# Kernel tuning notes

Measured on AMD Instinct MI355X. Metric: run time of the kernel, lower is better.

## Reference

```python
import jax, jax.numpy as jnp
import numpy as np

B, S = 32, 48
H, W_IMG, DEPTH = 48, 72, 1
UNITS, MOTOR, SENSORY = 48, 4, 1283
ODE_UNFOLDS = 6
N_ACTIONS = 2
EPS = 1e-8


def setup_inputs() -> dict:
    key = jax.random.key(0)
    ks = jax.random.split(key, 32)
    inp = {}
    inp["image"] = jax.random.uniform(ks[0], (B, S, DEPTH, H, W_IMG), jnp.float32)
    inp["rel_pos"] = jax.random.normal(ks[1], (B, S, 3), jnp.float32)
    # CNN params: channels [1->32->64->32], k=3, stride=2, VALID
    dims = [DEPTH, 32, 64, 32]
    for i in range(3):
        fan_in = dims[i] * 9
        inp[f"w{i}"] = jax.random.normal(ks[2 + i], (dims[i + 1], dims[i], 3, 3), jnp.float32) / np.sqrt(fan_in)
        inp[f"b{i}"] = jnp.zeros((dims[i + 1],), jnp.float32)
    # LTC input affine mapping
    inp["input_w"] = jnp.ones((SENSORY,), jnp.float32)
    inp["input_b"] = jnp.zeros((SENSORY,), jnp.float32)
    # LTC neuron params (ncps default init ranges)
    u = lambda k, shp, lo, hi: jax.random.uniform(k, shp, jnp.float32, lo, hi)
    inp["gleak"] = u(ks[6], (UNITS,), 0.001, 1.0)
    inp["vleak"] = u(ks[7], (UNITS,), -0.2, 0.2)
    inp["cm"] = u(ks[8], (UNITS,), 0.4, 0.6)
    # recurrent synapse params [pre=UNITS, post=UNITS]
    inp["sigma"] = u(ks[9], (UNITS, UNITS), 3.0, 8.0)
    inp["mu"] = u(ks[10], (UNITS, UNITS), 0.3, 0.8)
    inp["w_syn"] = u(ks[11], (UNITS, UNITS), 0.001, 1.0)
    inp["erev"] = (2.0 * jax.random.randint(ks[12], (UNITS, UNITS), 0, 2).astype(jnp.float32) - 1.0)
    # sensory synapse params [pre=SENSORY, post=UNITS]
    inp["s_sigma"] = u(ks[13], (SENSORY, UNITS), 3.0, 8.0)
    inp["s_mu"] = u(ks[14], (SENSORY, UNITS), 0.3, 0.8)
    inp["s_w"] = u(ks[15], (SENSORY, UNITS), 0.001, 1.0)
    inp["s_erev"] = (2.0 * jax.random.randint(ks[16], (SENSORY, UNITS), 0, 2).astype(jnp.float32) - 1.0)
    # output affine mapping over the 4 motor neurons
    inp["w_out"] = jnp.ones((MOTOR,), jnp.float32)
    inp["b_out"] = jnp.zeros((MOTOR,), jnp.float32)
    # actor head: Linear(4 -> n_actions) + tanh
    inp["w_head"] = jax.random.normal(ks[17], (MOTOR, N_ACTIONS), jnp.float32) / np.sqrt(MOTOR)
    inp["b_head"] = jnp.zeros((N_ACTIONS,), jnp.float32)
    # sparsity masks (buffers, non-trainable): AutoNCP-like sparse wiring
    inp["syn_mask"] = jax.random.randint(ks[18], (UNITS, UNITS), 0, 2, jnp.int32)
    inp["sens_mask"] = (jax.random.uniform(ks[19], (SENSORY, UNITS)) < 0.4).astype(jnp.int32)
    return inp


def _cnn(x, w0, b0, w1, b1, w2, b2):
    # x: [N, C, H, W], VALID padding, stride 2, ReLU
    for w, b in ((w0, b0), (w1, b1), (w2, b2)):
        x = jax.lax.conv_general_dilated(x, w, (2, 2), "VALID",
                                         dimension_numbers=("NCHW", "OIHW", "NCHW"))
        x = jax.nn.relu(x + b[None, :, None, None])
    return x


def _ltc(xs, input_w, input_b, gleak, vleak, cm, sigma, mu, w_syn, erev,
         s_sigma, s_mu, s_w, s_erev, w_out, b_out, syn_mask_f, sens_mask_f):
    # xs: [B, S, SENSORY] -> outputs [B, S, MOTOR]
    xs = xs * input_w + input_b  # input affine mapping
    cm_t = cm * ODE_UNFOLDS      # cm / (elapsed_time / ode_unfolds), elapsed=1

    def cell(v, x_t):
        # sensory synapse activation, computed once per step: [B, SENSORY, UNITS]
        sa = s_w * jax.nn.sigmoid((x_t[:, :, None] - s_mu) * s_sigma) * sens_mask_f
        w_num_s = jnp.sum(sa * s_erev, axis=1)  # [B, UNITS]
        w_den_s = jnp.sum(sa, axis=1)
        for _ in range(ODE_UNFOLDS):
            # recurrent synapse activation: [B, UNITS(pre), UNITS(post)]
            wa = w_syn * jax.nn.sigmoid((v[:, :, None] - mu) * sigma) * syn_mask_f
            num = cm_t * v + gleak * vleak + jnp.sum(wa * erev, axis=1) + w_num_s
            den = cm_t + gleak + jnp.sum(wa, axis=1) + w_den_s + EPS
            v = num / den
        out = v[:, :MOTOR] * w_out + b_out  # motor neurons + output affine
        return v, out

    v0 = jnp.zeros((xs.shape[0], UNITS), xs.dtype)
    _, outs = jax.lax.scan(cell, v0, jnp.swapaxes(xs, 0, 1))  # scan over time
    return jnp.swapaxes(outs, 0, 1)  # [B, S, MOTOR]


def reference(image, rel_pos, w0, b0, w1, b1, w2, b2, input_w, input_b,
              gleak, vleak, cm, sigma, mu, w_syn, erev,
              s_sigma, s_mu, s_w, s_erev, w_out, b_out, w_head, b_head,
              syn_mask, sens_mask):
    b, s = image.shape[0], image.shape[1]
    img = image.reshape(b * s, *image.shape[2:])
    feat = _cnn(img, w0, b0, w1, b1, w2, b2).reshape(b, s, -1)  # [B,S,1280]
    x = jnp.concatenate([feat, rel_pos.reshape(b, s, -1)], axis=2)  # [B,S,1283]
    outs = _ltc(x, input_w, input_b, gleak, vleak, cm, sigma, mu, w_syn, erev,
                s_sigma, s_mu, s_w, s_erev, w_out, b_out,
                syn_mask.astype(x.dtype), sens_mask.astype(x.dtype))
    pooled = outs.mean(axis=1)  # [B, MOTOR]
    return jnp.tanh(pooled @ w_head + b_head)  # [B, N_ACTIONS]
```

## Files before the change

### kernel.cpp

```cpp
#include <hip/hip_runtime.h>
#include <math.h>

#define DINL __device__ __forceinline__

typedef __attribute__((ext_vector_type(8))) short short8;
typedef __attribute__((ext_vector_type(4))) float f32x4;
typedef unsigned short ushortx;
typedef unsigned int uintx;


static constexpr int O_OUT2 = 0;
static constexpr int O_X    = O_OUT2 + 1536 * 187 * 64;
static constexpr int O_WNUM = O_X + 1536 * 1283;
static constexpr int O_WDEN = O_WNUM + 1536 * 48;
static constexpr int O_SP4  = O_WDEN + 1536 * 48;
static constexpr int O_WM   = O_SP4 + 4 * 48 * 1283;
static constexpr int O_WME  = O_WM + 48 * 48;
static constexpr int O_W2T  = O_WME + 48 * 48;
static constexpr int O_W1H  = O_W2T + 32 * 9 * 64;
static constexpr int O_W1L  = O_W1H + 9216;

DINL float sigmoid_f(float z) {
  return __builtin_amdgcn_rcpf(1.f + __expf(-z));
}

DINL ushortx bf16_rne(float x) {
  uintx u = __float_as_uint(x);
  return (ushortx)((u + 0x7FFFu + ((u >> 16) & 1u)) >> 16);
}

__global__ __launch_bounds__(256) void k_pre(
    const float* __restrict__ ssig, const float* __restrict__ smu,
    const float* __restrict__ sw, const float* __restrict__ serev,
    const int* __restrict__ smask,
    const float* __restrict__ w_syn, const float* __restrict__ erev,
    const int* __restrict__ syn_mask,
    const float* __restrict__ w1, const float* __restrict__ w2,
    float4* __restrict__ o_p4, float* __restrict__ o_wm, float* __restrict__ o_wme,
    float* __restrict__ w2t, ushortx* __restrict__ w1h, ushortx* __restrict__ w1l) {
  const int bid = blockIdx.x, t = threadIdx.x;
  if (bid < 241) {
    int idx = bid * 256 + t;
    if (idx < 61584) {
      int i = idx / 48, j = idx - i * 48;
      float m = (float)smask[idx];
      float w = sw[idx] * m;
      o_p4[j * 1283 + i] = make_float4(ssig[idx], smu[idx], w, w * serev[idx]);
    }
  } else if (bid < 250) {
    int idx = (bid - 241) * 256 + t;
    if (idx < 2304) {
      float wm = w_syn[idx] * (float)syn_mask[idx];
      o_wm[idx]  = wm;
      o_wme[idx] = wm * erev[idx];
    }
  } else {
    int idx = (bid - 250) * 256 + t;
    if (idx < 18432) {
      int oc = idx / 288;
      int rem = idx - oc * 288;
      int c = rem / 9, k = rem - c * 9;
      float v = w1[idx];
      ushortx h = bf16_rne(v);
      float hv = __uint_as_float(((uintx)h) << 16);
      ushortx l = bf16_rne(v - hv);
      int dst = (k * 64 + oc) * 32 + c;
      w1h[dst] = h;
      w1l[dst] = l;
    } else if (idx < 36864) {
      int i2 = idx - 18432;
      int oc = i2 / 576;
      int rem = i2 - oc * 576;
      int c = rem / 9, k = rem - c * 9;
      w2t[(((oc & 15) * 9 + k) * 64 + c) * 2 + (oc >> 4)] = w2[i2];
    }
  }
}

__global__ __launch_bounds__(512) void k_conv12(const float* __restrict__ gimg,
        const float* __restrict__ w0, const float* __restrict__ b0,
        const ushortx* __restrict__ w1h, const ushortx* __restrict__ w1l,
        const float* __restrict__ b1, float* __restrict__ gout2) {
  extern __shared__ __align__(16) char dyn[];
  ushortx* c1h = (ushortx*)dyn;
  ushortx* c1l = c1h + 26496;
  float* smem_a = (float*)(c1l + 26496);
  float* sw0 = smem_a + 3456;
  float* sb0 = sw0 + 288;
  ushortx* swh = (ushortx*)smem_a;
  ushortx* swl = swh + 2048;

  const int n = blockIdx.x, t = threadIdx.x;

  const float* gi = gimg + n * 3456;
  for (int k = t; k < 3456; k += 512) smem_a[k] = gi[k];
  if (t < 288) sw0[t] = w0[t];
  if (t >= 480) sb0[t - 480] = b0[t - 480];

  const int lane = t & 63, wid = t >> 6;
  const int r15 = lane & 15, kg = lane >> 4;
  const int mt0 = (wid & 1) * 2;
  const int nt0 = (wid >> 1) * 3;
  int bbase[3], spv[3];
#pragma unroll
  for (int ni = 0; ni < 3; ++ni) {
    int sp = (nt0 + ni) * 16 + r15;
    spv[ni] = sp;
    int spc = sp > 186 ? 186 : sp;
    int oh = spc / 17, ow = spc - oh * 17;
    bbase[ni] = ((2 * oh) * 36 + 2 * ow) * 32 + kg * 8;
  }
  int aoff0 = (mt0 * 16 + r15) * 32 + kg * 8;
  float4 bb[2];
  bb[0] = *(const float4*)(b1 + mt0 * 16 + kg * 4);
  bb[1] = *(const float4*)(b1 + (mt0 + 1) * 16 + kg * 4);
  f32x4 acc[2][3];
#pragma unroll
  for (int mi = 0; mi < 2; ++mi)
#pragma unroll
    for (int ni = 0; ni < 3; ++ni) acc[mi][ni] = (f32x4)(0.f);

  __syncthreads();

  for (int idx = t; idx < 25760; idx += 512) {
    int c = idx & 31, sp = idx >> 5;
    int oh = sp / 35, ow = sp - oh * 35;
    const float* ip = smem_a + (2 * oh) * 72 + 2 * ow;
    const float* wp = sw0 + c * 9;
    float a = sb0[c];
#pragma unroll
    for (int kh = 0; kh < 3; ++kh)
      a += ip[kh * 72 + 0] * wp[kh * 3 + 0] + ip[kh * 72 + 1] * wp[kh * 3 + 1]
         + ip[kh * 72 + 2] * wp[kh * 3 + 2];
    a = fmaxf(a, 0.f);
    ushortx h = bf16_rne(a);
    float hv = __uint_as_float(((uintx)h) << 16);
    ushortx l = bf16_rne(a - hv);
    int pos = (oh * 36 + ow) * 32 + c;
    c1h[pos] = h;
    c1l[pos] = l;
  }

  const uintx* gwh = (const uintx*)w1h;
  const uintx* gwl = (const uintx*)w1l;
  for (int tap = 0; tap < 9; ++tap) {
    __syncthreads();
    for (int k = t; k < 1024; k += 512) {
      ((uintx*)swh)[k] = gwh[tap * 1024 + k];
      ((uintx*)swl)[k] = gwl[tap * 1024 + k];
    }
    __syncthreads();
    const int kh = tap / 3, kw = tap - kh * 3;
    const int toff = (kh * 36 + kw) * 32;
    short8 ah[2], al[2];
    ah[0] = *(const short8*)(swh + aoff0);
    al[0] = *(const short8*)(swl + aoff0);
    ah[1] = *(const short8*)(swh + aoff0 + 512);
    al[1] = *(const short8*)(swl + aoff0 + 512);
#pragma unroll
    for (int ni = 0; ni < 3; ++ni) {
      short8 bh = *(const short8*)(c1h + bbase[ni] + toff);
      short8 bl = *(const short8*)(c1l + bbase[ni] + toff);
#pragma unroll
      for (int mi = 0; mi < 2; ++mi) {
        acc[mi][ni] = __builtin_amdgcn_mfma_f32_16x16x32_bf16(ah[mi], bh, acc[mi][ni], 0, 0, 0);
        acc[mi][ni] = __builtin_amdgcn_mfma_f32_16x16x32_bf16(al[mi], bh, acc[mi][ni], 0, 0, 0);
        acc[mi][ni] = __builtin_amdgcn_mfma_f32_16x16x32_bf16(ah[mi], bl, acc[mi][ni], 0, 0, 0);
      }
    }
  }

  float* go = gout2 + n * 11968;
#pragma unroll
  for (int mi = 0; mi < 2; ++mi)
#pragma unroll
    for (int ni = 0; ni < 3; ++ni) {
      if (spv[ni] < 187) {
        float4 v;
        v.x = fmaxf(acc[mi][ni][0] + bb[mi].x, 0.f);
        v.y = fmaxf(acc[mi][ni][1] + bb[mi].y, 0.f);
        v.z = fmaxf(acc[mi][ni][2] + bb[mi].z, 0.f);
        v.w = fmaxf(acc[mi][ni][3] + bb[mi].w, 0.f);
        *(float4*)(go + spv[ni] * 64 + (mt0 + mi) * 16 + kg * 4) = v;
      }
    }
}

__global__ __launch_bounds__(256, 4) void k_conv3(const float* __restrict__ gout2,
        const float* __restrict__ w2t, const float* __restrict__ b2,
        const float* __restrict__ grel, float* __restrict__ gx) {
  __shared__ __align__(16) float sin2g[16 * 198];
  __shared__ __align__(16) float sw2g[16 * 290];
  const int n = blockIdx.x, t = threadIdx.x;
  const float* gi = gout2 + n * 11968;

  const int oc = t & 15, g = t >> 4;
  float acc[3][2];
  int rowb[3];
#pragma unroll
  for (int q = 0; q < 3; ++q) {
    acc[q][0] = b2[oc]; acc[q][1] = b2[oc + 16];
    int sp = q * 16 + g; if (sp > 39) sp = 39;
    int oh = sp >> 3, ow = sp & 7;
    rowb[q] = (2 * oh) * 18 + 2 * ow;
  }

  for (int grp = 0; grp < 4; ++grp) {
    for (int idx = t; idx < 2992; idx += 256) {
      int sp = idx >> 4, c = idx & 15;
      int h = sp / 17, w = sp - h * 17;
      sin2g[c * 198 + h * 18 + w] = gi[sp * 64 + grp * 16 + c];
    }
    for (int idx = t; idx < 4608; idx += 256) {
      int ocq2 = idx / 288, r = idx - ocq2 * 288;
      int k = r >> 5;
      sw2g[ocq2 * 290 + r] = w2t[(ocq2 * 9 + k) * 128 + grp * 32 + (r & 31)];
    }
    __syncthreads();

    for (int c = 0; c < 16; ++c) {
      const float* cb = sin2g + c * 198;
      const float* wb = sw2g + oc * 290 + c * 2;
#pragma unroll
      for (int kh = 0; kh < 3; ++kh) {
        float2 wv0 = *(const float2*)(wb + (kh * 3 + 0) * 32);
        float2 wv1 = *(const float2*)(wb + (kh * 3 + 1) * 32);
        float2 wv2 = *(const float2*)(wb + (kh * 3 + 2) * 32);
#pragma unroll
        for (int q = 0; q < 3; ++q) {
          const float* p = cb + rowb[q] + kh * 18;
          float2 x01 = *(const float2*)p;
          float x2 = p[2];
          acc[q][0] += x01.x * wv0.x + x01.y * wv1.x + x2 * wv2.x;
          acc[q][1] += x01.x * wv0.y + x01.y * wv1.y + x2 * wv2.y;
        }
      }
    }
    __syncthreads();
  }

  float* xo = gx + n * 1283;
#pragma unroll
  for (int q = 0; q < 3; ++q) {
    int sp = q * 16 + g;
    if (sp < 40) {
      xo[oc * 40 + sp]        = fmaxf(acc[q][0], 0.f);
      xo[(oc + 16) * 40 + sp] = fmaxf(acc[q][1], 0.f);
    }
  }
  if (t < 3) xo[1280 + t] = grel[n * 3 + t];
}

__global__ __launch_bounds__(256) void k_sensory(const float* __restrict__ gx,
        const float* __restrict__ iw, const float* __restrict__ ib,
        const float4* __restrict__ p4,
        float* __restrict__ wnum, float* __restrict__ wden) {
  __shared__ float xs[4 * 1283];
  const int t = threadIdx.x, bid = blockIdx.x;
  const int bs0 = (bid >> 1) * 4;
  const int jbase = (bid & 1) * 24;
  for (int idx = t; idx < 4 * 1283; idx += 256) {
    int slot = idx / 1283, i = idx - slot * 1283;
    xs[idx] = gx[(bs0 + slot) * 1283 + i] * iw[i] + ib[i];
  }
  __syncthreads();
  const int w = t >> 6, l = t & 63;
  for (int jj = 0; jj < 6; ++jj) {
    int j = jbase + w * 6 + jj;
    const float4* pp = p4 + j * 1283;
    float an[4], ad[4];
#pragma unroll
    for (int s2 = 0; s2 < 4; ++s2) { an[s2] = 0.f; ad[s2] = 0.f; }
    for (int i = l; i < 1283; i += 64) {
      float4 P = pp[i];
#pragma unroll
      for (int s2 = 0; s2 < 4; ++s2) {
        float sg = sigmoid_f((xs[s2 * 1283 + i] - P.y) * P.x);
        an[s2] += P.w * sg;
        ad[s2] += P.z * sg;
      }
    }
#pragma unroll
    for (int off = 32; off; off >>= 1)
#pragma unroll
      for (int s2 = 0; s2 < 4; ++s2) {
        an[s2] += __shfl_xor(an[s2], off);
        ad[s2] += __shfl_xor(ad[s2], off);
      }
    if (l == 0) {
#pragma unroll
      for (int s2 = 0; s2 < 4; ++s2) {
        wnum[(bs0 + s2) * 48 + j] = an[s2];
        wden[(bs0 + s2) * 48 + j] = ad[s2];
      }
    }
  }
}

__global__ __launch_bounds__(384) void k_scan(const float* __restrict__ gmu,
        const float* __restrict__ gsig, const float* __restrict__ wm,
        const float* __restrict__ wme, const float* __restrict__ wnum,
        const float* __restrict__ wden, const float* __restrict__ gleak,
        const float* __restrict__ vleak, const float* __restrict__ cm,
        const float* __restrict__ w_out, const float* __restrict__ b_out,
        const float* __restrict__ w_head, const float* __restrict__ b_head,
        float* __restrict__ out) {
  __shared__ float4 sp4[48 * 49];
  __shared__ float vbuf[2][48];
  __shared__ float m4[4];
  const int t = threadIdx.x, b = blockIdx.x;
  for (int idx = t; idx < 2304; idx += 384) {
    int i = idx / 48, jx = idx - i * 48;
    sp4[i * 49 + jx] = make_float4(gmu[idx], gsig[idx], wm[idx], wme[idx]);
  }
  if (t < 48) { vbuf[0][t] = 0.f; vbuf[1][t] = 0.f; }
  __syncthreads();

  const int j = t >> 3, g = t & 7;
  const float cmt = cm[j] * 6.f;
  const float gl = gleak[j];
  const float glv = gl * vleak[j];
  float psum = 0.f;
  const float* pn = wnum + b * 2304 + j;
  const float* pd = wden + b * 2304 + j;

  for (int s = 0; s < 48; ++s) {
    float wns = pn[s * 48], wds = pd[s * 48];
#pragma unroll 1
    for (int u = 0; u < 6; ++u) {
      int cur = u & 1;
      float an = 0.f, ad = 0.f;
#pragma unroll
      for (int q = 0; q < 6; ++q) {
        int i = g * 6 + q;
        float vi = vbuf[cur][i];
        float4 P = sp4[i * 49 + j];
        float sg = sigmoid_f((vi - P.x) * P.y);
        an += P.w * sg;
        ad += P.z * sg;
      }
      an += __shfl_xor(an, 1); ad += __shfl_xor(ad, 1);
      an += __shfl_xor(an, 2); ad += __shfl_xor(ad, 2);
      an += __shfl_xor(an, 4); ad += __shfl_xor(ad, 4);
      if (g == 0) {
        float vj = vbuf[cur][j];
        float num = cmt * vj + glv + an + wns;
        float den = cmt + gl + ad + wds + 1e-8f;
        vbuf[cur ^ 1][j] = num / den;
      }
      __syncthreads();
    }
    if (g == 0 && j < 4) psum += vbuf[0][j];
  }
  if (g == 0 && j < 4) m4[j] = psum * (1.f / 48.f) * w_out[j] + b_out[j];
  __syncthreads();
  if (t < 2) {
    float a = b_head[t];
#pragma unroll
    for (int jm = 0; jm < 4; ++jm) a += m4[jm] * w_head[jm * 2 + t];
    out[b * 2 + t] = tanhf(a);
  }
}

extern "C" void kernel_launch(void* const* d_in, const int* in_sizes, int n_in,
                              void* d_out, int out_size, void* d_ws, size_t ws_size,
                              hipStream_t stream) {
  const float* image   = (const float*)d_in[0];
  const float* rel     = (const float*)d_in[1];
  const float* w0      = (const float*)d_in[2];
  const float* b0      = (const float*)d_in[3];
  const float* w1      = (const float*)d_in[4];
  const float* b1      = (const float*)d_in[5];
  const float* w2      = (const float*)d_in[6];
  const float* b2      = (const float*)d_in[7];
  const float* iw      = (const float*)d_in[8];
  const float* ib      = (const float*)d_in[9];
  const float* gleak   = (const float*)d_in[10];
  const float* vleak   = (const float*)d_in[11];
  const float* cm      = (const float*)d_in[12];
  const float* sigma   = (const float*)d_in[13];
  const float* mu      = (const float*)d_in[14];
  const float* w_syn   = (const float*)d_in[15];
  const float* erev    = (const float*)d_in[16];
  const float* s_sigma = (const float*)d_in[17];
  const float* s_mu    = (const float*)d_in[18];
  const float* s_w     = (const float*)d_in[19];
  const float* s_erev  = (const float*)d_in[20];
  const float* w_out   = (const float*)d_in[21];
  const float* b_out   = (const float*)d_in[22];
  const float* w_head  = (const float*)d_in[23];
  const float* b_head  = (const float*)d_in[24];
  const int* syn_mask  = (const int*)d_in[25];
  const int* sens_mask = (const int*)d_in[26];
  float* ws  = (float*)d_ws;
  float* out = (float*)d_out;

  hipFuncSetAttribute((const void*)k_conv12,
                      hipFuncAttributeMaxDynamicSharedMemorySize, 131072);

  k_pre<<<394, 256, 0, stream>>>(s_sigma, s_mu, s_w, s_erev, sens_mask,
      w_syn, erev, syn_mask, w1, w2,
      (float4*)(ws + O_SP4), ws + O_WM, ws + O_WME, ws + O_W2T,
      (ushortx*)(ws + O_W1H), (ushortx*)(ws + O_W1L));

  k_conv12<<<1536, 512, 121088, stream>>>(image, w0, b0,
      (const ushortx*)(ws + O_W1H), (const ushortx*)(ws + O_W1L), b1, ws + O_OUT2);
  k_conv3<<<1536, 256, 0, stream>>>(ws + O_OUT2, ws + O_W2T, b2, rel, ws + O_X);

  k_sensory<<<768, 256, 0, stream>>>(ws + O_X, iw, ib,
      (const float4*)(ws + O_SP4), ws + O_WNUM, ws + O_WDEN);

  k_scan<<<32, 384, 0, stream>>>(mu, sigma, ws + O_WM, ws + O_WME,
      ws + O_WNUM, ws + O_WDEN, gleak, vleak, cm,
      w_out, b_out, w_head, b_head, out);
}
```

Measured before the change: 522.1 us.

## Hold recurrent synapse params in registers and shrink scan block to 192 threads

The recurrent scan kernel now packs mu, sigma, masked weight and weight*erev into one float4 array during preprocessing. Each thread keeps its 12 presynaptic parameter sets in registers instead of reading them from shared memory on every ODE unfold. The block is halved to 192 threads with 4 lanes per neuron, which removes one shuffle level and reads the voltage buffer with vector loads. Per-step sensory inputs are staged into shared memory up front instead of being read from global memory inside the loop. This shortens the latency-bound serial loop, at the cost of more register pressure and less parallelism per neuron.

```diff
diff --git a/kernel.cpp b/kernel.cpp
--- a/kernel.cpp
+++ b/kernel.cpp
@@ -19,6 +19,7 @@
 static constexpr int O_W2T  = O_WME + 48 * 48;
 static constexpr int O_W1H  = O_W2T + 32 * 9 * 64;
 static constexpr int O_W1L  = O_W1H + 9216;
+static constexpr int O_R4   = O_W1L + 9216;
 
 DINL float sigmoid_f(float z) {
   return __builtin_amdgcn_rcpf(1.f + __expf(-z));
@@ -35,8 +36,9 @@
     const int* __restrict__ smask,
     const float* __restrict__ w_syn, const float* __restrict__ erev,
     const int* __restrict__ syn_mask,
+    const float* __restrict__ gmu, const float* __restrict__ gsig,
     const float* __restrict__ w1, const float* __restrict__ w2,
-    float4* __restrict__ o_p4, float* __restrict__ o_wm, float* __restrict__ o_wme,
+    float4* __restrict__ o_p4, float4* __restrict__ o_r4,
     float* __restrict__ w2t, ushortx* __restrict__ w1h, ushortx* __restrict__ w1l) {
   const int bid = blockIdx.x, t = threadIdx.x;
   if (bid < 241) {
@@ -51,8 +53,7 @@
     int idx = (bid - 241) * 256 + t;
     if (idx < 2304) {
       float wm = w_syn[idx] * (float)syn_mask[idx];
-      o_wm[idx]  = wm;
-      o_wme[idx] = wm * erev[idx];
+      o_r4[idx] = make_float4(gmu[idx], gsig[idx], wm, wm * erev[idx]);
     }
   } else {
     int idx = (bid - 250) * 256 + t;
@@ -297,51 +298,52 @@
   }
 }
 
-__global__ __launch_bounds__(384) void k_scan(const float* __restrict__ gmu,
-        const float* __restrict__ gsig, const float* __restrict__ wm,
-        const float* __restrict__ wme, const float* __restrict__ wnum,
-        const float* __restrict__ wden, const float* __restrict__ gleak,
-        const float* __restrict__ vleak, const float* __restrict__ cm,
+__global__ __launch_bounds__(192) void k_scan(const float4* __restrict__ r4,
+        const float* __restrict__ wnum, const float* __restrict__ wden,
+        const float* __restrict__ gleak, const float* __restrict__ vleak,
+        const float* __restrict__ cm,
         const float* __restrict__ w_out, const float* __restrict__ b_out,
         const float* __restrict__ w_head, const float* __restrict__ b_head,
         float* __restrict__ out) {
-  __shared__ float4 sp4[48 * 49];
-  __shared__ float vbuf[2][48];
+  __shared__ float swn[48 * 48], swd[48 * 48];
+  __shared__ __align__(16) float vbuf[2][48];
   __shared__ float m4[4];
   const int t = threadIdx.x, b = blockIdx.x;
-  for (int idx = t; idx < 2304; idx += 384) {
-    int i = idx / 48, jx = idx - i * 48;
-    sp4[i * 49 + jx] = make_float4(gmu[idx], gsig[idx], wm[idx], wme[idx]);
-  }
-  if (t < 48) { vbuf[0][t] = 0.f; vbuf[1][t] = 0.f; }
-  __syncthreads();
-
-  const int j = t >> 3, g = t & 7;
+  const int j = t >> 2, g = t & 3;
+
+  const float* gn = wnum + b * 2304;
+  const float* gd = wden + b * 2304;
+  for (int k = t; k < 2304; k += 192) { swn[k] = gn[k]; swd[k] = gd[k]; }
+
+  float4 P[12];
+#pragma unroll
+  for (int q = 0; q < 12; ++q) P[q] = r4[(g * 12 + q) * 48 + j];
+
   const float cmt = cm[j] * 6.f;
   const float gl = gleak[j];
   const float glv = gl * vleak[j];
+  if (t < 48) { vbuf[0][t] = 0.f; vbuf[1][t] = 0.f; }
   float psum = 0.f;
-  const float* pn = wnum + b * 2304 + j;
-  const float* pd = wden + b * 2304 + j;
-
+  __syncthreads();
+
+  int cur = 0;
   for (int s = 0; s < 48; ++s) {
-    float wns = pn[s * 48], wds = pd[s * 48];
+    float wns = swn[s * 48 + j], wds = swd[s * 48 + j];
 #pragma unroll 1
     for (int u = 0; u < 6; ++u) {
-      int cur = u & 1;
+      const float4* vb4 = (const float4*)&vbuf[cur][g * 12];
+      float4 va = vb4[0], vb = vb4[1], vc = vb4[2];
+      float vv[12] = {va.x, va.y, va.z, va.w, vb.x, vb.y, vb.z, vb.w,
+                      vc.x, vc.y, vc.z, vc.w};
       float an = 0.f, ad = 0.f;
 #pragma unroll
-      for (int q = 0; q < 6; ++q) {
-        int i = g * 6 + q;
-        float vi = vbuf[cur][i];
-        float4 P = sp4[i * 49 + j];
-        float sg = sigmoid_f((vi - P.x) * P.y);
-        an += P.w * sg;
-        ad += P.z * sg;
+      for (int q = 0; q < 12; ++q) {
+        float sg = sigmoid_f((vv[q] - P[q].x) * P[q].y);
+        an += P[q].w * sg;
+        ad += P[q].z * sg;
       }
       an += __shfl_xor(an, 1); ad += __shfl_xor(ad, 1);
       an += __shfl_xor(an, 2); ad += __shfl_xor(ad, 2);
-      an += __shfl_xor(an, 4); ad += __shfl_xor(ad, 4);
       if (g == 0) {
         float vj = vbuf[cur][j];
         float num = cmt * vj + glv + an + wns;
@@ -349,8 +351,9 @@
         vbuf[cur ^ 1][j] = num / den;
       }
       __syncthreads();
-    }
-    if (g == 0 && j < 4) psum += vbuf[0][j];
+      cur ^= 1;
+    }
+    if (g == 0 && j < 4) psum += vbuf[cur][j];
   }
   if (g == 0 && j < 4) m4[j] = psum * (1.f / 48.f) * w_out[j] + b_out[j];
   __syncthreads();
@@ -399,8 +402,8 @@
                       hipFuncAttributeMaxDynamicSharedMemorySize, 131072);
 
   k_pre<<<394, 256, 0, stream>>>(s_sigma, s_mu, s_w, s_erev, sens_mask,
-      w_syn, erev, syn_mask, w1, w2,
-      (float4*)(ws + O_SP4), ws + O_WM, ws + O_WME, ws + O_W2T,
+      w_syn, erev, syn_mask, mu, sigma, w1, w2,
+      (float4*)(ws + O_SP4), (float4*)(ws + O_R4), ws + O_W2T,
       (ushortx*)(ws + O_W1H), (ushortx*)(ws + O_W1L));
 
   k_conv12<<<1536, 512, 121088, stream>>>(image, w0, b0,
@@ -410,7 +413,7 @@
   k_sensory<<<768, 256, 0, stream>>>(ws + O_X, iw, ib,
       (const float4*)(ws + O_SP4), ws + O_WNUM, ws + O_WDEN);
 
-  k_scan<<<32, 384, 0, stream>>>(mu, sigma, ws + O_WM, ws + O_WME,
+  k_scan<<<32, 192, 0, stream>>>((const float4*)(ws + O_R4),
       ws + O_WNUM, ws + O_WDEN, gleak, vleak, cm,
       w_out, b_out, w_head, b_head, out);
 }
```

Result: no change. 512.0 us (-1.9%).
